# Performance work log

Measured on AMD Instinct MI355X. Metric: run time of the kernel, lower is better.

The kernel has to match this reference:

```python
import jax, jax.numpy as jnp
import numpy as np

HEADS = 8
HEAD_DIM = 32
DIM = 256        # embed_dim; inner_dim = HEADS*HEAD_DIM = 256
DEPTH = 2
MLP_DIM = 1024
GRID_H, GRID_W = 64, 64
CELL_DIM = 15    # pe(0) + in(3) + out(3) + hidden(9)
PE_IN = 3        # cell_pe_patch_dim + cell_in_patch_dim
UPDATE_DIM = 12  # cell_out(3) + hidden(9)
BATCH = 8


def layer_norm(x, g, b, eps=1e-5):
    m = jnp.mean(x, axis=-1, keepdims=True)
    v = jnp.var(x, axis=-1, keepdims=True)
    return (x - m) * jax.lax.rsqrt(v + eps) * g + b


def vit_positional_encoding(n, dim):
    pos = jnp.arange(n, dtype=jnp.float32)[:, None]
    div = jnp.exp(jnp.arange(0, dim, 2, dtype=jnp.float32) * (-np.log(10000.0) / dim))
    pe = jnp.zeros((n, dim), dtype=jnp.float32)
    pe = pe.at[:, 0::2].set(jnp.sin(pos * div)).at[:, 1::2].set(jnp.cos(pos * div))
    return pe[None]  # [1, n, dim]


def localize(x, H, W):
    # x: [b, heads, n, d] with n = H*W. Gather circular 3x3 neighbourhood per position
    # (equivalent to circular pad + one-hot conv in the torch LocalizeAttention).
    b, nh, n, d = x.shape
    y = x.reshape(b, nh, H, W, d)
    neigh = [jnp.roll(y, (1 - ki, 1 - kj), axis=(2, 3)) for ki in range(3) for kj in range(3)]
    return jnp.stack(neigh, axis=4).reshape(b, nh, n, 9, d)  # [b, h, n, 9, d]


def setup_inputs() -> dict:
    key = jax.random.key(0)
    ks = jax.random.split(key, 20)
    d = {}
    d['cells'] = jax.random.normal(ks[0], (BATCH, CELL_DIM, GRID_H, GRID_W), dtype=jnp.float32)
    s = 0.02
    d['We'] = jax.random.normal(ks[1], (CELL_DIM, DIM), jnp.float32) * s
    d['be'] = jnp.zeros((DIM,), jnp.float32)
    d['ln1_g'] = jnp.ones((DEPTH, DIM), jnp.float32)
    d['ln1_b'] = jnp.zeros((DEPTH, DIM), jnp.float32)
    d['Wqkv'] = jax.random.normal(ks[2], (DEPTH, DIM, 3 * HEADS * HEAD_DIM), jnp.float32) * s
    d['Wo'] = jax.random.normal(ks[3], (DEPTH, HEADS * HEAD_DIM, DIM), jnp.float32) * s
    d['bo'] = jnp.zeros((DEPTH, DIM), jnp.float32)
    d['ln2_g'] = jnp.ones((DEPTH, DIM), jnp.float32)
    d['ln2_b'] = jnp.zeros((DEPTH, DIM), jnp.float32)
    d['W1'] = jax.random.normal(ks[4], (DEPTH, DIM, MLP_DIM), jnp.float32) * s
    d['b1'] = jnp.zeros((DEPTH, MLP_DIM), jnp.float32)
    d['W2'] = jax.random.normal(ks[5], (DEPTH, MLP_DIM, DIM), jnp.float32) * s
    d['b2'] = jnp.zeros((DEPTH, DIM), jnp.float32)
    d['lnh_g'] = jnp.ones((DIM,), jnp.float32)
    d['lnh_b'] = jnp.zeros((DIM,), jnp.float32)
    # NOTE: torch zero-inits mlp_head; we use small random weights so the output is nontrivial.
    d['Wh'] = jax.random.normal(ks[6], (DIM, UPDATE_DIM), jnp.float32) * s
    d['bh'] = jnp.zeros((UPDATE_DIM,), jnp.float32)
    return d


def reference(cells, We, be, ln1_g, ln1_b, Wqkv, Wo, bo, ln2_g, ln2_b,
              W1, b1, W2, b2, lnh_g, lnh_b, Wh, bh):
    b, c, H, W = cells.shape
    n = H * W
    x = cells.reshape(b, c, n).transpose(0, 2, 1)           # b n c
    x = x @ We + be                                         # cell_to_embedding
    x = x + vit_positional_encoding(n, x.shape[-1])
    scale = HEAD_DIM ** -0.5
    for l in range(DEPTH):
        y = layer_norm(x, ln1_g[l], ln1_b[l])
        qkv = y @ Wqkv[l]                                   # b n 3*inner
        q, k, v = jnp.split(qkv, 3, axis=-1)
        split_heads = lambda t: t.reshape(b, n, HEADS, HEAD_DIM).transpose(0, 2, 1, 3)
        q, k, v = split_heads(q), split_heads(k), split_heads(v)  # b h n d
        kl = localize(k, H, W)                              # b h n 9 d
        vl = localize(v, H, W)
        dots = jnp.einsum('bhnd,bhnkd->bhnk', q, kl) * scale
        attn = jax.nn.softmax(dots, axis=-1)
        out = jnp.einsum('bhnk,bhnkd->bhnd', attn, vl)
        out = out.transpose(0, 2, 1, 3).reshape(b, n, HEADS * HEAD_DIM)
        x = out @ Wo[l] + bo[l] + x                         # attention + residual
        y = layer_norm(x, ln2_g[l], ln2_b[l])
        y = jax.nn.gelu(y @ W1[l] + b1[l], approximate=False) @ W2[l] + b2[l]
        x = x + y                                           # ffn + residual
    upd = layer_norm(x, lnh_g, lnh_b) @ Wh + bh             # b n UPDATE_DIM
    upd = upd.transpose(0, 2, 1).reshape(b, UPDATE_DIM, H, W)
    # update_rate = 1.0 -> deterministic branch: cells[:, PE_IN:] + update
    updated = cells[:, PE_IN:] + upd
    return jnp.concatenate([cells[:, :PE_IN], updated], axis=1)
```

## Files before the change

### kernel.cpp

```cpp
#include <hip/hip_runtime.h>
#include <hip/hip_bf16.h>
#include <math.h>

#define HEADS 8
#define HEAD_DIM 32
#define DIM 256
#define MLP_DIM 1024
#define NTOK 4096
#define BATCH 8
#define M_TOK (BATCH*NTOK)
#define CELL_DIM 15
#define PE_IN 3
#define UPD 12
#define HME ((size_t)M_TOK*32)

typedef __attribute__((ext_vector_type(8))) short bf16x8;
typedef __attribute__((ext_vector_type(4))) float f32x4;

static __device__ __forceinline__ unsigned short f2bf(float f) {
    __hip_bfloat16 h = __float2bfloat16(f);
    union { __hip_bfloat16 h; unsigned short u; } cv; cv.h = h; return cv.u;
}
static __device__ __forceinline__ void gload_lds16(const unsigned short* g, unsigned short* l) {
    __builtin_amdgcn_global_load_lds(
        (const __attribute__((address_space(1))) void*)g,
        (__attribute__((address_space(3))) void*)l, 16, 0, 0);
}
static __device__ __forceinline__ float gelu_fast(float v) {
    return v / (1.f + __expf(-1.59576912f * (v + 0.044715f * v * v * v)));
}

__global__ __launch_bounds__(256) void k_embed(const float* __restrict__ cells,
        const float* __restrict__ We, const float* __restrict__ be,
        const float* __restrict__ g, const float* __restrict__ bln,
        float* __restrict__ x, unsigned short* __restrict__ y) {
    __shared__ float red[8];
    int tok = blockIdx.x;
    int d = threadIdx.x;
    int b = tok >> 12, n = tok & 4095;
    const float* cb = cells + (size_t)b * CELL_DIM * NTOK + n;
    float acc = 0.f;
#pragma unroll
    for (int c = 0; c < CELL_DIM; ++c)
        acc += cb[c * NTOK] * We[c * DIM + d];
    int i = d >> 1;
    float freq = __expf(-0.03597789f * (float)(2 * i));
    float ph = (float)n * freq;
    float pe = (d & 1) ? __cosf(ph) : __sinf(ph);
    float v = acc + be[d] + pe;
    x[(size_t)tok * DIM + d] = v;
    float s = v, ss = v * v;
#pragma unroll
    for (int off = 32; off; off >>= 1) { s += __shfl_xor(s, off); ss += __shfl_xor(ss, off); }
    int wave = d >> 6, lane = d & 63;
    if (lane == 0) { red[wave] = s; red[4 + wave] = ss; }
    __syncthreads();
    float stot = red[0] + red[1] + red[2] + red[3];
    float sstot = red[4] + red[5] + red[6] + red[7];
    float mean = stot * (1.f / DIM);
    float rstd = rsqrtf(sstot * (1.f / DIM) - mean * mean + 1e-5f);
    y[(size_t)tok * DIM + d] = f2bf((v - mean) * rstd * g[d] + bln[d]);
}

__global__ __launch_bounds__(256) void k_prep(const float* __restrict__ Wqkv,
        const float* __restrict__ Wo, const float* __restrict__ W1,
        const float* __restrict__ W2, const float* __restrict__ Wh,
        unsigned short* __restrict__ wT) {
    int seg = blockIdx.y;
    int idx = blockIdx.x * 256 + threadIdx.x;
    if (seg == 8) {
        if (idx >= 16 * 256) return;
        int u = idx >> 8, k = idx & 255;
        wT[1572864 + idx] = (u < UPD) ? f2bf(Wh[(size_t)k * UPD + u]) : (unsigned short)0;
        return;
    }
    int l = seg >> 2, mat = seg & 3;
    const float* src; int kwSh, Nw; size_t ooff;
    switch (mat) {
        case 0: src = Wqkv + (size_t)l * 196608; kwSh = 8;  Nw = 768;  ooff = (size_t)l * 786432 + 0;      break;
        case 1: src = Wo   + (size_t)l * 65536;  kwSh = 8;  Nw = 256;  ooff = (size_t)l * 786432 + 196608; break;
        case 2: src = W1   + (size_t)l * 262144; kwSh = 8;  Nw = 1024; ooff = (size_t)l * 786432 + 262144; break;
        default:src = W2   + (size_t)l * 262144; kwSh = 10; Nw = 256;  ooff = (size_t)l * 786432 + 524288; break;
    }
    int Kw = 1 << kwSh;
    if (idx >= Kw * Nw) return;
    int n = idx >> kwSh, k = idx & (Kw - 1);
    wT[ooff + idx] = f2bf(src[(size_t)k * Nw + n]);
}

template<int EPI, int KT>
__global__ __launch_bounds__(256) void k_mgemm(const unsigned short* __restrict__ A,
        const unsigned short* __restrict__ BT, const float* __restrict__ bias,
        void* __restrict__ Cout, int M, int N, int NT) {
    __shared__ unsigned short As[4][128 * 32];
    __shared__ unsigned short Bs[4][128 * 32];
    int bid = blockIdx.x;
    int cpx = gridDim.x >> 3;
    int sb = (bid & 7) * cpx + (bid >> 3);
    int mt = sb / NT, nt = sb - mt * NT;
    int m0 = mt * 128, n0 = nt * 128;
    int t = threadIdx.x;
    int lane = t & 63, w = t >> 6;
    int wm = (w >> 1) * 64, wn = (w & 1) * 64;
    f32x4 acc[4][4] = {};
    int srow = t >> 2;
    int cg = (t & 3) ^ ((srow >> 1) & 3);
    const unsigned short* aBase = A  + (size_t)(m0 + srow) * KT + cg * 8;
    const unsigned short* bBase = BT + (size_t)(n0 + srow) * KT + cg * 8;
    int fr = lane & 15, kb8 = lane >> 4;

    auto stage = [&](int buf, int k0) {
        unsigned short* a = &As[0][0] + buf * 4096;
        unsigned short* b = &Bs[0][0] + buf * 4096;
        gload_lds16(aBase + k0,           a + t * 8);
        gload_lds16(aBase + 64 * KT + k0, a + 2048 + t * 8);
        gload_lds16(bBase + k0,           b + t * 8);
        gload_lds16(bBase + 64 * KT + k0, b + 2048 + t * 8);
    };
    auto compute = [&](int buf) {
        const unsigned short* a = &As[0][0] + buf * 4096;
        const unsigned short* b = &Bs[0][0] + buf * 4096;
        bf16x8 af[4], bfv[4];
#pragma unroll
        for (int i = 0; i < 4; ++i) {
            int r_ = wm + i * 16 + fr;
            af[i] = *(const bf16x8*)&a[r_ * 32 + ((kb8 ^ ((r_ >> 1) & 3)) << 3)];
        }
#pragma unroll
        for (int j = 0; j < 4; ++j) {
            int r_ = wn + j * 16 + fr;
            bfv[j] = *(const bf16x8*)&b[r_ * 32 + ((kb8 ^ ((r_ >> 1) & 3)) << 3)];
        }
        __builtin_amdgcn_s_setprio(1);
#pragma unroll
        for (int i = 0; i < 4; ++i)
#pragma unroll
            for (int j = 0; j < 4; ++j)
                acc[i][j] = __builtin_amdgcn_mfma_f32_16x16x32_bf16(bfv[j], af[i], acc[i][j], 0, 0, 0);
        __builtin_amdgcn_s_setprio(0);
    };

    constexpr int NK = KT >> 5;
    stage(0, 0);
    stage(1, 32);
    stage(2, 64);
    asm volatile("s_waitcnt vmcnt(8)" ::: "memory");
    __builtin_amdgcn_s_barrier();
    __builtin_amdgcn_sched_barrier(0);
#pragma unroll
    for (int k = 0; k < NK - 1; ++k) {
        if (k + 3 < NK) stage((k + 3) & 3, (k + 3) * 32);
        compute(k & 3);
        __builtin_amdgcn_sched_barrier(0);
        if (k + 3 < NK)      asm volatile("s_waitcnt vmcnt(8)" ::: "memory");
        else if (k + 2 < NK) asm volatile("s_waitcnt vmcnt(4)" ::: "memory");
        else                 asm volatile("s_waitcnt vmcnt(0)" ::: "memory");
        __builtin_amdgcn_s_barrier();
        __builtin_amdgcn_sched_barrier(0);
    }
    compute((NK - 1) & 3);

    int mcol = lane & 15, nq = (lane >> 4) * 4;
#pragma unroll
    for (int i = 0; i < 4; ++i) {
        int m = m0 + wm + i * 16 + mcol;
#pragma unroll
        for (int j = 0; j < 4; ++j) {
            int ng = n0 + wn + j * 16 + nq;
            if (EPI == 3) {
                int type = ng >> 8, rem = ng & 255;
                ushort4 pk;
                pk.x = f2bf(acc[i][j][0]); pk.y = f2bf(acc[i][j][1]);
                pk.z = f2bf(acc[i][j][2]); pk.w = f2bf(acc[i][j][3]);
                *(ushort4*)((unsigned short*)Cout +
                    (size_t)(type * 8 + (rem >> 5)) * HME + (size_t)m * 32 + (rem & 31)) = pk;
            } else {
                float4 b4 = *(const float4*)&bias[ng];
                ushort4 pk;
                pk.x = f2bf(gelu_fast(acc[i][j][0] + b4.x));
                pk.y = f2bf(gelu_fast(acc[i][j][1] + b4.y));
                pk.z = f2bf(gelu_fast(acc[i][j][2] + b4.z));
                pk.w = f2bf(gelu_fast(acc[i][j][3] + b4.w));
                *(ushort4*)((unsigned short*)Cout + (size_t)m * N + ng) = pk;
            }
        }
    }
}

template<int ALAYOUT>
__global__ __launch_bounds__(256, 2) void k_mgemm_ln(const unsigned short* __restrict__ A,
        const unsigned short* __restrict__ BT, const float* __restrict__ bias,
        const float* __restrict__ g, const float* __restrict__ bln,
        float* __restrict__ x, unsigned short* __restrict__ y, int K) {
    __shared__ unsigned short As[3][64 * 32];
    __shared__ unsigned short Bs[3][256 * 32];
    __shared__ float sred[64 * 4];
    __shared__ float ssred[64 * 4];
    __shared__ float msr[64 * 2];
    int t = threadIdx.x;
    int lane = t & 63, w = t >> 6;
    int wn = w * 64;
    int m0 = blockIdx.x * 64;
    int mloc = lane & 15, nq = (lane >> 4) * 4;

    float4 xres[4][4];
#pragma unroll
    for (int i = 0; i < 4; ++i) {
        int gm = m0 + i * 16 + mloc;
#pragma unroll
        for (int j = 0; j < 4; ++j)
            xres[i][j] = *(const float4*)&x[(size_t)gm * DIM + wn + j * 16 + nq];
    }
    __builtin_amdgcn_sched_barrier(0);

    f32x4 acc[4][4] = {};
    int srow = t >> 2;
    int cg = (t & 3) ^ ((srow >> 1) & 3);
    const unsigned short* aBase = (ALAYOUT == 0)
        ? A + (size_t)(m0 + srow) * K + cg * 8
        : A + (size_t)(m0 + srow) * 32 + cg * 8;
    const unsigned short* bBase = BT + (size_t)srow * K + cg * 8;
    int fr = lane & 15, kb8 = lane >> 4;

    auto stage = [&](int buf, int k0) {
        unsigned short* as_ = &As[0][0] + buf * 2048;
        unsigned short* bs_ = &Bs[0][0] + buf * 8192;
        const unsigned short* aSrc = (ALAYOUT == 0) ? aBase + k0 : aBase + (size_t)(k0 >> 5) * HME;
        gload_lds16(aSrc, as_ + t * 8);
#pragma unroll
        for (int i = 0; i < 4; ++i)
            gload_lds16(bBase + (size_t)(64 * i) * K + k0, bs_ + i * 2048 + t * 8);
    };
    auto compute = [&](int buf) {
        const unsigned short* as_ = &As[0][0] + buf * 2048;
        const unsigned short* bs_ = &Bs[0][0] + buf * 8192 + w * 2048;
        bf16x8 af[4], bfv[4];
#pragma unroll
        for (int i = 0; i < 4; ++i) {
            int r_ = i * 16 + fr;
            af[i] = *(const bf16x8*)&as_[r_ * 32 + ((kb8 ^ ((r_ >> 1) & 3)) << 3)];
        }
#pragma unroll
        for (int j = 0; j < 4; ++j) {
            int rl = j * 16 + fr;
            bfv[j] = *(const bf16x8*)&bs_[rl * 32 + ((kb8 ^ ((rl >> 1) & 3)) << 3)];
        }
#pragma unroll
        for (int i = 0; i < 4; ++i)
#pragma unroll
            for (int j = 0; j < 4; ++j)
                acc[i][j] = __builtin_amdgcn_mfma_f32_16x16x32_bf16(bfv[j], af[i], acc[i][j], 0, 0, 0);
    };

    int nk = K >> 5;
    stage(0, 0);
    stage(1, 32);
    asm volatile("s_waitcnt vmcnt(5)" ::: "memory");
    __builtin_amdgcn_s_barrier();
    __builtin_amdgcn_sched_barrier(0);
    int cur = 0;
    for (int k = 0; k < nk - 1; ++k) {
        int pre = k + 2;
        if (pre < nk) {
            int preBuf = cur + 2; if (preBuf >= 3) preBuf -= 3;
            stage(preBuf, pre * 32);
        }
        compute(cur);
        __builtin_amdgcn_sched_barrier(0);
        if (pre < nk) asm volatile("s_waitcnt vmcnt(5)" ::: "memory");
        else          asm volatile("s_waitcnt vmcnt(0)" ::: "memory");
        __builtin_amdgcn_s_barrier();
        __builtin_amdgcn_sched_barrier(0);
        ++cur; if (cur >= 3) cur -= 3;
    }
    compute(cur);

#pragma unroll
    for (int i = 0; i < 4; ++i) {
        float s = 0.f, ss = 0.f;
#pragma unroll
        for (int j = 0; j < 4; ++j) {
            int nb = wn + j * 16 + nq;
            float4 b4 = *(const float4*)&bias[nb];
            acc[i][j][0] += b4.x + xres[i][j].x;
            acc[i][j][1] += b4.y + xres[i][j].y;
            acc[i][j][2] += b4.z + xres[i][j].z;
            acc[i][j][3] += b4.w + xres[i][j].w;
#pragma unroll
            for (int r = 0; r < 4; ++r) { float v = acc[i][j][r]; s += v; ss += v * v; }
        }
        s += __shfl_xor(s, 16); ss += __shfl_xor(ss, 16);
        s += __shfl_xor(s, 32); ss += __shfl_xor(ss, 32);
        if (lane < 16) {
            int row = i * 16 + lane;
            sred[row * 4 + w] = s;
            ssred[row * 4 + w] = ss;
        }
    }
    __syncthreads();
    if (t < 64) {
        float s = sred[t * 4] + sred[t * 4 + 1] + sred[t * 4 + 2] + sred[t * 4 + 3];
        float ss = ssred[t * 4] + ssred[t * 4 + 1] + ssred[t * 4 + 2] + ssred[t * 4 + 3];
        float mean = s * (1.f / DIM);
        float var = ss * (1.f / DIM) - mean * mean;
        msr[t * 2] = mean;
        msr[t * 2 + 1] = rsqrtf(var + 1e-5f);
    }
    __syncthreads();
#pragma unroll
    for (int i = 0; i < 4; ++i) {
        int row = i * 16 + mloc;
        int gm = m0 + row;
        float mean = msr[row * 2], rstd = msr[row * 2 + 1];
#pragma unroll
        for (int j = 0; j < 4; ++j) {
            int nb = wn + j * 16 + nq;
            float4 gv4 = *(const float4*)&g[nb];
            float4 bb4 = *(const float4*)&bln[nb];
            float4 xo;
            xo.x = acc[i][j][0]; xo.y = acc[i][j][1];
            xo.z = acc[i][j][2]; xo.w = acc[i][j][3];
            *(float4*)&x[(size_t)gm * DIM + nb] = xo;
            ushort4 yv;
            yv.x = f2bf((xo.x - mean) * rstd * gv4.x + bb4.x);
            yv.y = f2bf((xo.y - mean) * rstd * gv4.y + bb4.y);
            yv.z = f2bf((xo.z - mean) * rstd * gv4.z + bb4.z);
            yv.w = f2bf((xo.w - mean) * rstd * gv4.w + bb4.w);
            *(ushort4*)&y[(size_t)gm * DIM + nb] = yv;
        }
    }
}

__global__ __launch_bounds__(256) void k_attn(const unsigned short* __restrict__ qkvH,
        unsigned short* __restrict__ attnH) {
    int t = threadIdx.x;
    int h = t >> 5, tl = t & 31;
    int tok = blockIdx.x * 32 + tl;
    int b = tok >> 12, n = tok & 4095;
    int r = n >> 6, c = n & 63;

    float q[32];
    {
        const uint4* u = (const uint4*)(qkvH + (size_t)h * HME + (size_t)tok * 32);
#pragma unroll
        for (int i = 0; i < 4; ++i) {
            uint4 x4 = u[i];
            unsigned wv[4] = {x4.x, x4.y, x4.z, x4.w};
#pragma unroll
            for (int wj = 0; wj < 4; ++wj) {
                q[i * 8 + wj * 2]     = __uint_as_float(wv[wj] << 16);
                q[i * 8 + wj * 2 + 1] = __uint_as_float(wv[wj] & 0xffff0000u);
            }
        }
    }
    int nts[9];
    float dots[9];
    const unsigned short* kbase = qkvH + (size_t)(8 + h) * HME;
#pragma unroll
    for (int ki = 0; ki < 3; ++ki)
#pragma unroll
        for (int kj = 0; kj < 3; ++kj) {
            int rr = (r + ki - 1) & 63, cc = (c + kj - 1) & 63;
            int nt = (b << 12) + (rr << 6) + cc;
            nts[ki * 3 + kj] = nt;
            const uint4* u = (const uint4*)(kbase + (size_t)nt * 32);
            float acc = 0.f;
#pragma unroll
            for (int i = 0; i < 4; ++i) {
                uint4 x4 = u[i];
                unsigned wv[4] = {x4.x, x4.y, x4.z, x4.w};
#pragma unroll
                for (int wj = 0; wj < 4; ++wj) {
                    acc += __uint_as_float(wv[wj] << 16)        * q[i * 8 + wj * 2];
                    acc += __uint_as_float(wv[wj] & 0xffff0000u) * q[i * 8 + wj * 2 + 1];
                }
            }
            dots[ki * 3 + kj] = acc * 0.17677669529f;
        }
    float m = dots[0];
#pragma unroll
    for (int j = 1; j < 9; ++j) m = fmaxf(m, dots[j]);
    float sum = 0.f;
#pragma unroll
    for (int j = 0; j < 9; ++j) { dots[j] = __expf(dots[j] - m); sum += dots[j]; }
    float inv = 1.f / sum;
    float o[32] = {};
    const unsigned short* vbase = qkvH + (size_t)(16 + h) * HME;
#pragma unroll
    for (int j = 0; j < 9; ++j) {
        float wgt = dots[j] * inv;
        const uint4* u = (const uint4*)(vbase + (size_t)nts[j] * 32);
#pragma unroll
        for (int i = 0; i < 4; ++i) {
            uint4 x4 = u[i];
            unsigned wv[4] = {x4.x, x4.y, x4.z, x4.w};
#pragma unroll
            for (int wj = 0; wj < 4; ++wj) {
                o[i * 8 + wj * 2]     += wgt * __uint_as_float(wv[wj] << 16);
                o[i * 8 + wj * 2 + 1] += wgt * __uint_as_float(wv[wj] & 0xffff0000u);
            }
        }
    }
    uint4 st[4];
    unsigned* sw = (unsigned*)st;
#pragma unroll
    for (int i = 0; i < 16; ++i)
        sw[i] = (unsigned)f2bf(o[2 * i]) | ((unsigned)f2bf(o[2 * i + 1]) << 16);
    uint4* od = (uint4*)(attnH + (size_t)h * HME + (size_t)tok * 32);
#pragma unroll
    for (int i = 0; i < 4; ++i) od[i] = st[i];
}

__global__ __launch_bounds__(256) void k_headgemv(const unsigned short* __restrict__ y,
        const unsigned short* __restrict__ WhT, float* __restrict__ Cg) {
    int t = threadIdx.x, lane = t & 63, w = t >> 6;
    int m0 = blockIdx.x * 64 + w * 16;
    int fr = lane & 15, kb = (lane >> 4) * 8;
    f32x4 acc = {};
    const unsigned short* aRow = y + (size_t)(m0 + fr) * DIM + kb;
    const unsigned short* bRow = WhT + (size_t)fr * DIM + kb;
#pragma unroll
    for (int k0 = 0; k0 < DIM; k0 += 32) {
        bf16x8 a = *(const bf16x8*)(aRow + k0);
        bf16x8 bfr = *(const bf16x8*)(bRow + k0);
        acc = __builtin_amdgcn_mfma_f32_16x16x32_bf16(a, bfr, acc, 0, 0, 0);
    }
    int col = lane & 15, rowq = (lane >> 4) * 4;
#pragma unroll
    for (int r = 0; r < 4; ++r)
        Cg[(size_t)(m0 + rowq + r) * 16 + col] = acc[r];
}

__global__ __launch_bounds__(256) void k_assemble(const float* __restrict__ cells,
        const float* __restrict__ Cg, const float* __restrict__ bh,
        float* __restrict__ outp) {
    int idx = blockIdx.x * 256 + threadIdx.x;
    int total = BATCH * CELL_DIM * (NTOK / 4);
    if (idx >= total) return;
    int n4 = idx & 1023;
    int c = (idx >> 10) % CELL_DIM;
    int b = idx / (CELL_DIM * 1024);
    size_t ci = ((size_t)b * CELL_DIM + c) * NTOK + n4 * 4;
    float4 o = *(const float4*)(cells + ci);
    if (c >= PE_IN) {
        int u = c - PE_IN;
        float bias = bh[u];
        size_t tok = (size_t)b * NTOK + n4 * 4;
        o.x += Cg[(tok + 0) * 16 + u] + bias;
        o.y += Cg[(tok + 1) * 16 + u] + bias;
        o.z += Cg[(tok + 2) * 16 + u] + bias;
        o.w += Cg[(tok + 3) * 16 + u] + bias;
    }
    *(float4*)(outp + ci) = o;
}

extern "C" void kernel_launch(void* const* d_in, const int* in_sizes, int n_in,
                              void* d_out, int out_size, void* d_ws, size_t ws_size,
                              hipStream_t stream) {
    const float* cells = (const float*)d_in[0];
    const float* We    = (const float*)d_in[1];
    const float* be    = (const float*)d_in[2];
    const float* ln1_g = (const float*)d_in[3];
    const float* ln1_b = (const float*)d_in[4];
    const float* Wqkv  = (const float*)d_in[5];
    const float* Wo    = (const float*)d_in[6];
    const float* bo    = (const float*)d_in[7];
    const float* ln2_g = (const float*)d_in[8];
    const float* ln2_b = (const float*)d_in[9];
    const float* W1    = (const float*)d_in[10];
    const float* b1    = (const float*)d_in[11];
    const float* W2    = (const float*)d_in[12];
    const float* b2    = (const float*)d_in[13];
    const float* lnh_g = (const float*)d_in[14];
    const float* lnh_b = (const float*)d_in[15];
    const float* Wh    = (const float*)d_in[16];
    const float* bh    = (const float*)d_in[17];
    float* outp = (float*)d_out;

    char* ws = (char*)d_ws;
    float* x = (float*)ws;
    unsigned short* y = (unsigned short*)(ws + 33554432);
    unsigned short* scratch = (unsigned short*)(ws + 50331648);
    unsigned short* wT = (unsigned short*)(ws + 117440512);
    unsigned short* qkvH  = scratch;
    unsigned short* attnH = scratch + 24 * HME;
    unsigned short* hidden = scratch;
    float* Cg = (float*)scratch;

    k_prep<<<dim3(1024, 9), 256, 0, stream>>>(Wqkv, Wo, W1, W2, Wh, wT);
    k_embed<<<M_TOK, 256, 0, stream>>>(cells, We, be, ln1_g, ln1_b, x, y);
    for (int l = 0; l < 2; ++l) {
        const unsigned short* wL = wT + (size_t)l * 786432;
        const float* gN = (l == 0) ? ln1_g + DIM : lnh_g;
        const float* bN = (l == 0) ? ln1_b + DIM : lnh_b;
        k_mgemm<3, 256><<<1536, 256, 0, stream>>>(
            y, wL + 0, nullptr, qkvH, M_TOK, 768, 6);
        k_attn<<<M_TOK / 32, 256, 0, stream>>>(qkvH, attnH);
        k_mgemm_ln<1><<<M_TOK / 64, 256, 0, stream>>>(
            attnH, wL + 196608, bo + l * DIM, ln2_g + l * DIM, ln2_b + l * DIM, x, y, DIM);
        k_mgemm<1, 256><<<2048, 256, 0, stream>>>(
            y, wL + 262144, b1 + l * MLP_DIM, hidden, M_TOK, MLP_DIM, 8);
        k_mgemm_ln<0><<<M_TOK / 64, 256, 0, stream>>>(
            hidden, wL + 524288, b2 + l * DIM, gN, bN, x, y, MLP_DIM);
    }
    k_headgemv<<<M_TOK / 64, 256, 0, stream>>>(y, wT + 1572864, Cg);
    k_assemble<<<(BATCH * CELL_DIM * (NTOK / 4) + 255) / 256, 256, 0, stream>>>(cells, Cg, bh, outp);
}
```

Baseline: 381.9 us.

## Use 8-wave blocks with halved per-wave N tiles in the GEMM kernels

Both the plain GEMM and the GEMM+LayerNorm kernels now launch 512 threads per block. Each wave computes a 64x32 (or 4x2 MFMA) sub-tile instead of 64x64, and global-to-LDS staging is redistributed across the larger thread count, with vmcnt waits adjusted to match. The LN kernel reuses the A staging buffer for its reduction scratch and pads its load count with a redundant B load so every thread issues the same number of loads. The aim is more waves in flight and lower register pressure per wave, to hide latency better. In exchange each wave does more LDS fragment reads per MFMA and has less register-level reuse.

```diff
diff --git a/kernel.cpp b/kernel.cpp
--- a/kernel.cpp
+++ b/kernel.cpp
@@ -89,7 +89,7 @@
 }
 
 template<int EPI, int KT>
-__global__ __launch_bounds__(256) void k_mgemm(const unsigned short* __restrict__ A,
+__global__ __launch_bounds__(512, 4) void k_mgemm(const unsigned short* __restrict__ A,
         const unsigned short* __restrict__ BT, const float* __restrict__ bias,
         void* __restrict__ Cout, int M, int N, int NT) {
     __shared__ unsigned short As[4][128 * 32];
@@ -101,8 +101,8 @@
     int m0 = mt * 128, n0 = nt * 128;
     int t = threadIdx.x;
     int lane = t & 63, w = t >> 6;
-    int wm = (w >> 1) * 64, wn = (w & 1) * 64;
-    f32x4 acc[4][4] = {};
+    int wm = (w >> 2) * 64, wn = (w & 3) * 32;
+    f32x4 acc[4][2] = {};
     int srow = t >> 2;
     int cg = (t & 3) ^ ((srow >> 1) & 3);
     const unsigned short* aBase = A  + (size_t)(m0 + srow) * KT + cg * 8;
@@ -110,24 +110,20 @@
     int fr = lane & 15, kb8 = lane >> 4;
 
     auto stage = [&](int buf, int k0) {
-        unsigned short* a = &As[0][0] + buf * 4096;
-        unsigned short* b = &Bs[0][0] + buf * 4096;
-        gload_lds16(aBase + k0,           a + t * 8);
-        gload_lds16(aBase + 64 * KT + k0, a + 2048 + t * 8);
-        gload_lds16(bBase + k0,           b + t * 8);
-        gload_lds16(bBase + 64 * KT + k0, b + 2048 + t * 8);
+        gload_lds16(aBase + k0, &As[0][0] + buf * 4096 + t * 8);
+        gload_lds16(bBase + k0, &Bs[0][0] + buf * 4096 + t * 8);
     };
     auto compute = [&](int buf) {
         const unsigned short* a = &As[0][0] + buf * 4096;
         const unsigned short* b = &Bs[0][0] + buf * 4096;
-        bf16x8 af[4], bfv[4];
+        bf16x8 af[4], bfv[2];
 #pragma unroll
         for (int i = 0; i < 4; ++i) {
             int r_ = wm + i * 16 + fr;
             af[i] = *(const bf16x8*)&a[r_ * 32 + ((kb8 ^ ((r_ >> 1) & 3)) << 3)];
         }
 #pragma unroll
-        for (int j = 0; j < 4; ++j) {
+        for (int j = 0; j < 2; ++j) {
             int r_ = wn + j * 16 + fr;
             bfv[j] = *(const bf16x8*)&b[r_ * 32 + ((kb8 ^ ((r_ >> 1) & 3)) << 3)];
         }
@@ -135,7 +131,7 @@
 #pragma unroll
         for (int i = 0; i < 4; ++i)
 #pragma unroll
-            for (int j = 0; j < 4; ++j)
+            for (int j = 0; j < 2; ++j)
                 acc[i][j] = __builtin_amdgcn_mfma_f32_16x16x32_bf16(bfv[j], af[i], acc[i][j], 0, 0, 0);
         __builtin_amdgcn_s_setprio(0);
     };
@@ -144,7 +140,7 @@
     stage(0, 0);
     stage(1, 32);
     stage(2, 64);
-    asm volatile("s_waitcnt vmcnt(8)" ::: "memory");
+    asm volatile("s_waitcnt vmcnt(4)" ::: "memory");
     __builtin_amdgcn_s_barrier();
     __builtin_amdgcn_sched_barrier(0);
 #pragma unroll
@@ -152,8 +148,8 @@
         if (k + 3 < NK) stage((k + 3) & 3, (k + 3) * 32);
         compute(k & 3);
         __builtin_amdgcn_sched_barrier(0);
-        if (k + 3 < NK)      asm volatile("s_waitcnt vmcnt(8)" ::: "memory");
-        else if (k + 2 < NK) asm volatile("s_waitcnt vmcnt(4)" ::: "memory");
+        if (k + 3 < NK)      asm volatile("s_waitcnt vmcnt(4)" ::: "memory");
+        else if (k + 2 < NK) asm volatile("s_waitcnt vmcnt(2)" ::: "memory");
         else                 asm volatile("s_waitcnt vmcnt(0)" ::: "memory");
         __builtin_amdgcn_s_barrier();
         __builtin_amdgcn_sched_barrier(0);
@@ -165,7 +161,7 @@
     for (int i = 0; i < 4; ++i) {
         int m = m0 + wm + i * 16 + mcol;
 #pragma unroll
-        for (int j = 0; j < 4; ++j) {
+        for (int j = 0; j < 2; ++j) {
             int ng = n0 + wn + j * 16 + nq;
             if (EPI == 3) {
                 int type = ng >> 8, rem = ng & 255;
@@ -188,74 +184,83 @@
 }
 
 template<int ALAYOUT>
-__global__ __launch_bounds__(256, 2) void k_mgemm_ln(const unsigned short* __restrict__ A,
+__global__ __launch_bounds__(512, 4) void k_mgemm_ln(const unsigned short* __restrict__ A,
         const unsigned short* __restrict__ BT, const float* __restrict__ bias,
         const float* __restrict__ g, const float* __restrict__ bln,
         float* __restrict__ x, unsigned short* __restrict__ y, int K) {
     __shared__ unsigned short As[3][64 * 32];
     __shared__ unsigned short Bs[3][256 * 32];
-    __shared__ float sred[64 * 4];
-    __shared__ float ssred[64 * 4];
-    __shared__ float msr[64 * 2];
+    float* sred = (float*)&As[0][0];
+    float* ssred = sred + 512;
+    float* msr = ssred + 512;
     int t = threadIdx.x;
     int lane = t & 63, w = t >> 6;
-    int wn = w * 64;
+    int wn = w * 32;
     int m0 = blockIdx.x * 64;
     int mloc = lane & 15, nq = (lane >> 4) * 4;
 
-    float4 xres[4][4];
+    float4 xres[4][2];
 #pragma unroll
     for (int i = 0; i < 4; ++i) {
         int gm = m0 + i * 16 + mloc;
 #pragma unroll
-        for (int j = 0; j < 4; ++j)
+        for (int j = 0; j < 2; ++j)
             xres[i][j] = *(const float4*)&x[(size_t)gm * DIM + wn + j * 16 + nq];
     }
     __builtin_amdgcn_sched_barrier(0);
 
-    f32x4 acc[4][4] = {};
-    int srow = t >> 2;
-    int cg = (t & 3) ^ ((srow >> 1) & 3);
+    f32x4 acc[4][2] = {};
+    int rB0 = t >> 2, cgB0 = (t & 3) ^ ((rB0 >> 1) & 3);
+    int c1 = t + 512;
+    int rB1 = c1 >> 2, cgB1 = (c1 & 3) ^ ((rB1 >> 1) & 3);
+    int tA = t & 255;
+    int rA = tA >> 2, cgA = (tA & 3) ^ ((rA >> 1) & 3);
     const unsigned short* aBase = (ALAYOUT == 0)
-        ? A + (size_t)(m0 + srow) * K + cg * 8
-        : A + (size_t)(m0 + srow) * 32 + cg * 8;
-    const unsigned short* bBase = BT + (size_t)srow * K + cg * 8;
+        ? A + (size_t)(m0 + rA) * K + cgA * 8
+        : A + (size_t)(m0 + rA) * 32 + cgA * 8;
+    const unsigned short* b0Base = BT + (size_t)rB0 * K + cgB0 * 8;
+    const unsigned short* b1Base = BT + (size_t)rB1 * K + cgB1 * 8;
     int fr = lane & 15, kb8 = lane >> 4;
 
     auto stage = [&](int buf, int k0) {
         unsigned short* as_ = &As[0][0] + buf * 2048;
         unsigned short* bs_ = &Bs[0][0] + buf * 8192;
-        const unsigned short* aSrc = (ALAYOUT == 0) ? aBase + k0 : aBase + (size_t)(k0 >> 5) * HME;
-        gload_lds16(aSrc, as_ + t * 8);
-#pragma unroll
-        for (int i = 0; i < 4; ++i)
-            gload_lds16(bBase + (size_t)(64 * i) * K + k0, bs_ + i * 2048 + t * 8);
+        gload_lds16(b0Base + k0, bs_ + t * 8);
+        gload_lds16(b1Base + k0, bs_ + 4096 + t * 8);
+        if (t < 256) {
+            const unsigned short* aSrc = (ALAYOUT == 0) ? aBase + k0 : aBase + (size_t)(k0 >> 5) * HME;
+            gload_lds16(aSrc, as_ + tA * 8);
+        } else {
+            gload_lds16(b0Base + k0, bs_ + t * 8);
+        }
     };
     auto compute = [&](int buf) {
         const unsigned short* as_ = &As[0][0] + buf * 2048;
-        const unsigned short* bs_ = &Bs[0][0] + buf * 8192 + w * 2048;
-        bf16x8 af[4], bfv[4];
+        const unsigned short* bs_ = &Bs[0][0] + buf * 8192;
+        bf16x8 af[4], bfv[2];
 #pragma unroll
         for (int i = 0; i < 4; ++i) {
             int r_ = i * 16 + fr;
             af[i] = *(const bf16x8*)&as_[r_ * 32 + ((kb8 ^ ((r_ >> 1) & 3)) << 3)];
         }
 #pragma unroll
-        for (int j = 0; j < 4; ++j) {
-            int rl = j * 16 + fr;
+        for (int j = 0; j < 2; ++j) {
+            int rl = wn + j * 16 + fr;
             bfv[j] = *(const bf16x8*)&bs_[rl * 32 + ((kb8 ^ ((rl >> 1) & 3)) << 3)];
         }
+        __builtin_amdgcn_s_setprio(1);
 #pragma unroll
         for (int i = 0; i < 4; ++i)
 #pragma unroll
-            for (int j = 0; j < 4; ++j)
+            for (int j = 0; j < 2; ++j)
                 acc[i][j] = __builtin_amdgcn_mfma_f32_16x16x32_bf16(bfv[j], af[i], acc[i][j], 0, 0, 0);
+        __builtin_amdgcn_s_setprio(0);
     };
 
     int nk = K >> 5;
     stage(0, 0);
     stage(1, 32);
-    asm volatile("s_waitcnt vmcnt(5)" ::: "memory");
+    asm volatile("s_waitcnt vmcnt(3)" ::: "memory");
     __builtin_amdgcn_s_barrier();
     __builtin_amdgcn_sched_barrier(0);
     int cur = 0;
@@ -267,19 +272,20 @@
         }
         compute(cur);
         __builtin_amdgcn_sched_barrier(0);
-        if (pre < nk) asm volatile("s_waitcnt vmcnt(5)" ::: "memory");
+        if (pre < nk) asm volatile("s_waitcnt vmcnt(3)" ::: "memory");
         else          asm volatile("s_waitcnt vmcnt(0)" ::: "memory");
         __builtin_amdgcn_s_barrier();
         __builtin_amdgcn_sched_barrier(0);
         ++cur; if (cur >= 3) cur -= 3;
     }
     compute(cur);
+    __syncthreads();
 
 #pragma unroll
     for (int i = 0; i < 4; ++i) {
         float s = 0.f, ss = 0.f;
 #pragma unroll
-        for (int j = 0; j < 4; ++j) {
+        for (int j = 0; j < 2; ++j) {
             int nb = wn + j * 16 + nq;
             float4 b4 = *(const float4*)&bias[nb];
             acc[i][j][0] += b4.x + xres[i][j].x;
@@ -293,14 +299,15 @@
         s += __shfl_xor(s, 32); ss += __shfl_xor(ss, 32);
         if (lane < 16) {
             int row = i * 16 + lane;
-            sred[row * 4 + w] = s;
-            ssred[row * 4 + w] = ss;
+            sred[row * 8 + w] = s;
+            ssred[row * 8 + w] = ss;
         }
     }
     __syncthreads();
     if (t < 64) {
-        float s = sred[t * 4] + sred[t * 4 + 1] + sred[t * 4 + 2] + sred[t * 4 + 3];
-        float ss = ssred[t * 4] + ssred[t * 4 + 1] + ssred[t * 4 + 2] + ssred[t * 4 + 3];
+        float s = 0.f, ss = 0.f;
+#pragma unroll
+        for (int q = 0; q < 8; ++q) { s += sred[t * 8 + q]; ss += ssred[t * 8 + q]; }
         float mean = s * (1.f / DIM);
         float var = ss * (1.f / DIM) - mean * mean;
         msr[t * 2] = mean;
@@ -313,7 +320,7 @@
         int gm = m0 + row;
         float mean = msr[row * 2], rstd = msr[row * 2 + 1];
 #pragma unroll
-        for (int j = 0; j < 4; ++j) {
+        for (int j = 0; j < 2; ++j) {
             int nb = wn + j * 16 + nq;
             float4 gv4 = *(const float4*)&g[nb];
             float4 bb4 = *(const float4*)&bln[nb];
@@ -493,14 +500,14 @@
         const unsigned short* wL = wT + (size_t)l * 786432;
         const float* gN = (l == 0) ? ln1_g + DIM : lnh_g;
         const float* bN = (l == 0) ? ln1_b + DIM : lnh_b;
-        k_mgemm<3, 256><<<1536, 256, 0, stream>>>(
+        k_mgemm<3, 256><<<1536, 512, 0, stream>>>(
             y, wL + 0, nullptr, qkvH, M_TOK, 768, 6);
         k_attn<<<M_TOK / 32, 256, 0, stream>>>(qkvH, attnH);
-        k_mgemm_ln<1><<<M_TOK / 64, 256, 0, stream>>>(
+        k_mgemm_ln<1><<<M_TOK / 64, 512, 0, stream>>>(
             attnH, wL + 196608, bo + l * DIM, ln2_g + l * DIM, ln2_b + l * DIM, x, y, DIM);
-        k_mgemm<1, 256><<<2048, 256, 0, stream>>>(
+        k_mgemm<1, 256><<<2048, 512, 0, stream>>>(
             y, wL + 262144, b1 + l * MLP_DIM, hidden, M_TOK, MLP_DIM, 8);
-        k_mgemm_ln<0><<<M_TOK / 64, 256, 0, stream>>>(
+        k_mgemm_ln<0><<<M_TOK / 64, 512, 0, stream>>>(
             hidden, wL + 524288, b2 + l * DIM, gN, bN, x, y, MLP_DIM);
     }
     k_headgemv<<<M_TOK / 64, 256, 0, stream>>>(y, wT + 1572864, Cg);
```

After: 371.2 us. 2.8% less time.
